# Optimization experiments

Measured on AMD Instinct MI355X. Metric: run time of the kernel, lower is better.

Reference implementation:

```python
import jax, jax.numpy as jnp
import numpy as np
import math

SCALE = 64.0
MARGIN = 0.5
EPS = 1e-07
COS_M = math.cos(MARGIN)
SIN_M = math.sin(MARGIN)
THRESHOLD = math.cos(math.pi - MARGIN)
MM = math.sin(math.pi - MARGIN) * MARGIN

N, D, C = 512, 512, 100000


def setup_inputs() -> dict:
    key = jax.random.key(0)
    k1, k2, k3 = jax.random.split(key, 3)
    x = jax.random.normal(k1, (N, D), dtype=jnp.float32)
    weight = jax.random.normal(k2, (C, D), dtype=jnp.float32)
    t = jnp.zeros((1,), dtype=jnp.float32)
    target = jax.random.randint(k3, (N,), 0, C, dtype=jnp.int64)
    return {"x": x, "weight": weight, "t": t, "target": target}


def reference(x, weight, t, target):
    # normalized linear -> cosine similarities [N, C]
    xn = x / jnp.linalg.norm(x, axis=1, keepdims=True)
    wn = weight / jnp.linalg.norm(weight, axis=1, keepdims=True)
    cos_theta = jnp.clip(jnp.einsum('nd,cd->nc', xn, wn), -1.0 + EPS, 1.0 - EPS)

    rows = jnp.arange(cos_theta.shape[0])
    target_logit = cos_theta[rows, target][:, None]            # [N, 1]
    sin_theta = jnp.sqrt(1.0 - target_logit * target_logit)
    cos_theta_m = target_logit * COS_M - sin_theta * SIN_M      # cos(theta + m)

    mask = cos_theta > cos_theta_m                              # hard examples
    final_target_logit = jnp.where(target_logit > THRESHOLD,
                                   cos_theta_m,
                                   target_logit - MM)

    # EMA buffer update (no-grad in torch)
    t_new = jax.lax.stop_gradient(target_logit.mean() * 0.01 + 0.99 * t)  # [1]

    # hard-example re-weighting: cos * (t + cos) where mask
    cos_theta = jnp.where(mask, cos_theta * (t_new[0] + cos_theta), cos_theta)
    # scatter margin-adjusted target logit into target column
    cos_theta = cos_theta.at[rows, target].set(final_target_logit[:, 0])

    logits = cos_theta * SCALE
    # cross entropy (mean)
    logp = jax.nn.log_softmax(logits, axis=-1)
    loss = -jnp.mean(logp[rows, target])
    return loss
```

## Files before the change

kernel.cpp:

```cpp
#include <hip/hip_runtime.h>
#include <hip/hip_bf16.h>
#include <stdint.h>

#define N_ROWS 512
#define D_DIM  512
#define C_CLS  100000

#define SCALE_F    64.0f
#define EPS_F      1e-7f
#define COS_M_F    0.8775825618903728f
#define SIN_M_F    0.4794255386042030f
#define THRESH_F  -0.8775825618903728f
#define MM_F       0.2397127693021015f
#define FIXMAX_F   65.0f

#define NC  64
#define NG2 1564

#define XN8_OFF    0
#define TL_OFF     (XN8_OFF + 512*512)
#define CTM_OFF    (TL_OFF + 2048)
#define FTL_OFF    (CTM_OFF + 2048)
#define TNEW_OFF   (FTL_OFF + 2048)
#define XNORM_OFF  (TNEW_OFF + 256)
#define PSUM_OFF   (XNORM_OFF + 2048)
#define LOSSI_OFF  (PSUM_OFF + NG2*512*4)

typedef __attribute__((ext_vector_type(4))) float f32x4;

#define GLOAD_LDS16(gp, lp) \
    __builtin_amdgcn_global_load_lds((const __attribute__((address_space(1))) void*)(gp), \
                                     (__attribute__((address_space(3))) void*)(lp), 16, 0, 0)

#if defined(__has_builtin)
#if __has_builtin(__builtin_amdgcn_cvt_pk_fp8_f32)
#define HAVE_CVT_FP8 1
#endif
#endif

__device__ inline unsigned char f2e4m3(float f) {
    union { float f; unsigned u; } a; a.f = f;
    unsigned s = (a.u >> 24) & 0x80u;
    float af = fabsf(f);
    if (af < 0.015625f) {
        int q = (int)(af * 512.0f + 0.5f);
        return (unsigned char)(s | (unsigned)q);
    }
    unsigned x = a.u & 0x7FFFFFFFu;
    unsigned r = x + 0x000FFFFFu + ((x >> 20) & 1u);
    int ec = (int)(r >> 23) - 127 + 7;
    unsigned m = (r >> 20) & 7u;
    if (ec > 15 || (ec == 15 && m == 7u)) return (unsigned char)(s | 0x7Eu);
    return (unsigned char)(s | ((unsigned)ec << 3) | m);
}

__device__ inline unsigned pack4_fp8(float f0, float f1, float f2, float f3) {
#ifdef HAVE_CVT_FP8
    int q = __builtin_amdgcn_cvt_pk_fp8_f32(f0, f1, 0, false);
    q     = __builtin_amdgcn_cvt_pk_fp8_f32(f2, f3, q, true);
    return (unsigned)q;
#else
    union { unsigned char b[4]; unsigned u; } u;
    u.b[0]=f2e4m3(f0); u.b[1]=f2e4m3(f1); u.b[2]=f2e4m3(f2); u.b[3]=f2e4m3(f3);
    return u.u;
#endif
}

__device__ inline uint2 pack8_fp8(float f0, float f1, float f2, float f3,
                                  float f4, float f5, float f6, float f7) {
    uint2 r;
    r.x = pack4_fp8(f0, f1, f2, f3);
    r.y = pack4_fp8(f4, f5, f6, f7);
    return r;
}

__device__ inline float wave_sum64(float v) {
    #pragma unroll
    for (int m = 1; m < 64; m <<= 1) v += __shfl_xor(v, m);
    return v;
}

__global__ void k_xnorm_fp8(const float* __restrict__ x,
                            unsigned char* __restrict__ xn8,
                            float* __restrict__ xnorm) {
    int row = blockIdx.x;
    int lane = threadIdx.x;
    const float* xr = x + row * D_DIM + lane * 8;
    float4 v0 = *(const float4*)(xr);
    float4 v1 = *(const float4*)(xr + 4);
    float s = v0.x*v0.x + v0.y*v0.y + v0.z*v0.z + v0.w*v0.w
            + v1.x*v1.x + v1.y*v1.y + v1.z*v1.z + v1.w*v1.w;
    s = wave_sum64(s);
    float nrm = sqrtf(s);
    if (lane == 0) xnorm[row] = nrm;
    float inv = 1.0f / nrm;
    uint2 q = pack8_fp8(v0.x*inv, v0.y*inv, v0.z*inv, v0.w*inv,
                        v1.x*inv, v1.y*inv, v1.z*inv, v1.w*inv);
    *(uint2*)(xn8 + row * D_DIM + lane * 8) = q;
}

__global__ void k_tlogit(const float* __restrict__ x, const float* __restrict__ w,
                         const float* __restrict__ xnorm,
                         const int* __restrict__ target,
                         float* __restrict__ tl, float* __restrict__ ctm,
                         float* __restrict__ ftl) {
    int row = blockIdx.x;
    int lane = threadIdx.x;
    int tgt = target[row];
    const float* xr = x + row * D_DIM + lane * 8;
    const float* wr = w + (size_t)tgt * D_DIM + lane * 8;
    float4 a0 = *(const float4*)(xr),     a1 = *(const float4*)(xr + 4);
    float4 b0 = *(const float4*)(wr),     b1 = *(const float4*)(wr + 4);
    float s = a0.x*b0.x + a0.y*b0.y + a0.z*b0.z + a0.w*b0.w
            + a1.x*b1.x + a1.y*b1.y + a1.z*b1.z + a1.w*b1.w;
    float q = b0.x*b0.x + b0.y*b0.y + b0.z*b0.z + b0.w*b0.w
            + b1.x*b1.x + b1.y*b1.y + b1.z*b1.z + b1.w*b1.w;
    s = wave_sum64(s);
    q = wave_sum64(q);
    if (lane == 0) {
        float c = s / (xnorm[row] * sqrtf(q));
        c = fminf(fmaxf(c, -1.0f + EPS_F), 1.0f - EPS_F);
        float sn = sqrtf(fmaxf(1.0f - c * c, 0.0f));
        float cm = c * COS_M_F - sn * SIN_M_F;
        tl[row]  = c;
        ctm[row] = cm;
        ftl[row] = (c > THRESH_F) ? cm : (c - MM_F);
    }
}

__global__ void k_tnew(const float* __restrict__ tl, const float* __restrict__ t,
                       float* __restrict__ tnew) {
    __shared__ float s[512];
    int tid = threadIdx.x;
    s[tid] = tl[tid];
    __syncthreads();
    for (int off = 256; off > 0; off >>= 1) {
        if (tid < off) s[tid] += s[tid + off];
        __syncthreads();
    }
    if (tid == 0) tnew[0] = (s[0] / 512.0f) * 0.01f + 0.99f * t[0];
}

__global__ __launch_bounds__(512, 4) void k_fused(
        const unsigned char* __restrict__ xn8,
        const float* __restrict__ w,
        const int* __restrict__ target,
        const float* __restrict__ ctm,
        const float* __restrict__ ftl,
        const float* __restrict__ tnew,
        float* __restrict__ psum) {
    __shared__ unsigned char As[2][512 * 32];
    __shared__ unsigned char Bs[2][64 * 32];
    __shared__ float invS[64];
    __shared__ int   tgt_s[512];
    __shared__ float ctm_s[512];
    __shared__ float ftl_s[512];

    int bx = blockIdx.x;
    int cb = bx * NC;
    int tid = threadIdx.x;
    int lane = tid & 63, wid = tid >> 6;
    int fr = lane & 15, rgrp = lane >> 4;
    int wrow = wid * 64;

    tgt_s[tid] = target[tid];
    ctm_s[tid] = ctm[tid];
    ftl_s[tid] = ftl[tid];
    float tn = tnew[0];

    int brow  = tid >> 3;
    int bslot = tid & 7;
    int bclass = cb + brow;
    bool brvalid = (bclass < C_CLS);
    const float* bsrc = w + (size_t)(brvalid ? bclass : 0) * D_DIM + bslot * 4;

    float sumsq = 0.0f;

    #define STAGE_A(kk, buf)                                                  \
        do {                                                                  \
            _Pragma("unroll")                                                 \
            for (int c = 0; c < 2; ++c) {                                     \
                int lo = c * 8192 + wid * 1024;             \
                int o  = lo + lane * 16;                                      \
                int row = o >> 5, b = o & 31;                                 \
                GLOAD_LDS16(xn8 + (size_t)row * 512 + (kk) * 32 + b,          \
                            (char*)As[buf] + lo);                             \
            }                                                                 \
        } while (0)

    #define WRITE_B(vv, buf)                                                  \
        do {                                                                  \
            sumsq += vv.x*vv.x + vv.y*vv.y + vv.z*vv.z + vv.w*vv.w;           \
            *(unsigned*)(&Bs[buf][brow * 32 + bslot * 4]) =                   \
                pack4_fp8(vv.x, vv.y, vv.z, vv.w);                            \
        } while (0)

    __builtin_amdgcn_sched_barrier(0);
    float4 v0 = *(const float4*)(bsrc);
    STAGE_A(0, 0);
    __builtin_amdgcn_sched_barrier(0);
    float4 rv_next = *(const float4*)(bsrc + 1 * 32);
    float4 rv_far  = *(const float4*)(bsrc + 2 * 32);
    WRITE_B(v0, 0);
    asm volatile("s_waitcnt vmcnt(2) lgkmcnt(0)" ::: "memory");
    __builtin_amdgcn_sched_barrier(0);
    __builtin_amdgcn_s_barrier();
    __builtin_amdgcn_sched_barrier(0);

    f32x4 acc[4][4];
    #pragma unroll
    for (int m = 0; m < 4; m++)
        #pragma unroll
        for (int j = 0; j < 4; j++)
            acc[m][j] = (f32x4){0.f, 0.f, 0.f, 0.f};

    union LL { uint2 u; long long ll; };

    #pragma unroll
    for (int kk = 0; kk < 16; ++kk) {
        int cur = kk & 1;
        if (kk < 15) {
            STAGE_A(kk + 1, cur ^ 1);
            __builtin_amdgcn_sched_barrier(0);
            WRITE_B(rv_next, cur ^ 1);
            rv_next = rv_far;
            if (kk < 13)
                rv_far = *(const float4*)(bsrc + (kk + 3) * 32);
        }
        uint2 af[4], bf[4];
        #pragma unroll
        for (int m = 0; m < 4; m++)
            af[m] = *(const uint2*)(&As[cur][(wrow + m * 16 + fr) * 32 + rgrp * 8]);
        #pragma unroll
        for (int j = 0; j < 4; j++)
            bf[j] = *(const uint2*)(&Bs[cur][(j * 16 + fr) * 32 + rgrp * 8]);
        __builtin_amdgcn_s_setprio(1);
        #pragma unroll
        for (int m = 0; m < 4; m++)
            #pragma unroll
            for (int j = 0; j < 4; j++) {
                LL a, b;
                a.u = af[m];
                b.u = bf[j];
                acc[m][j] = __builtin_amdgcn_mfma_f32_16x16x32_fp8_fp8(
                                a.ll, b.ll, acc[m][j], 0, 0, 0);
            }
        __builtin_amdgcn_s_setprio(0);
        if (kk < 15) {
            if (kk < 13)
                asm volatile("s_waitcnt vmcnt(1) lgkmcnt(0)" ::: "memory");
            else
                asm volatile("s_waitcnt vmcnt(0) lgkmcnt(0)" ::: "memory");
            __builtin_amdgcn_sched_barrier(0);
            __builtin_amdgcn_s_barrier();
            __builtin_amdgcn_sched_barrier(0);
        }
    }
    #undef STAGE_A
    #undef WRITE_B

    float s2 = sumsq;
    s2 += __shfl_xor(s2, 1);
    s2 += __shfl_xor(s2, 2);
    s2 += __shfl_xor(s2, 4);
    if (bslot == 0) invS[brow] = rsqrtf(s2);
    __syncthreads();

    float inv[4];
    bool cvalid[4];
    #pragma unroll
    for (int j = 0; j < 4; j++) {
        inv[j] = invS[j * 16 + fr];
        cvalid[j] = (cb + j * 16 + fr) < C_CLS;
    }
    #pragma unroll
    for (int m = 0; m < 4; m++) {
        #pragma unroll
        for (int reg = 0; reg < 4; reg++) {
            int rl = wrow + m * 16 + rgrp * 4 + reg;
            int tr = tgt_s[rl];
            float cm = ctm_s[rl];
            float ft = ftl_s[rl];
            float sm = 0.0f;
            #pragma unroll
            for (int j = 0; j < 4; j++) {
                int col = cb + j * 16 + fr;
                float c = acc[m][j][reg] * inv[j];
                c = fminf(fmaxf(c, -1.0f + EPS_F), 1.0f - EPS_F);
                float v = (c > cm) ? c * (tn + c) : c;
                v *= SCALE_F;
                v = (col == tr) ? ft * SCALE_F : v;
                v = cvalid[j] ? v : -3.0e38f;
                sm += __expf(v - FIXMAX_F);
            }
            #pragma unroll
            for (int msk = 1; msk < 16; msk <<= 1) sm += __shfl_xor(sm, msk);
            if (fr == 0) psum[(size_t)bx * 512 + rl] = sm;
        }
    }
}

__global__ void k_rowlse_fix(const float* __restrict__ psum,
                             const float* __restrict__ ftl,
                             float* __restrict__ lossi) {
    int row = blockIdx.x, tid = threadIdx.x;
    float S = 0.0f;
    for (int nb = tid; nb < NG2; nb += 256) S += psum[(size_t)nb * 512 + row];
    __shared__ float sS[256];
    sS[tid] = S;
    __syncthreads();
    for (int off = 128; off > 0; off >>= 1) {
        if (tid < off) sS[tid] += sS[tid + off];
        __syncthreads();
    }
    if (tid == 0) lossi[row] = logf(sS[0]) + FIXMAX_F - SCALE_F * ftl[row];
}

__global__ void k_final(const float* __restrict__ lossi, float* __restrict__ out) {
    __shared__ float s[512];
    int tid = threadIdx.x;
    s[tid] = lossi[tid];
    __syncthreads();
    for (int off = 256; off > 0; off >>= 1) {
        if (tid < off) s[tid] += s[tid + off];
        __syncthreads();
    }
    if (tid == 0) out[0] = s[0] / 512.0f;
}

extern "C" void kernel_launch(void* const* d_in, const int* in_sizes, int n_in,
                              void* d_out, int out_size, void* d_ws, size_t ws_size,
                              hipStream_t stream) {
    const float* x      = (const float*)d_in[0];
    const float* w      = (const float*)d_in[1];
    const float* t      = (const float*)d_in[2];
    const int*   target = (const int*)d_in[3];

    char* ws = (char*)d_ws;
    unsigned char* xn8  = (unsigned char*)(ws + XN8_OFF);
    float* tl    = (float*)(ws + TL_OFF);
    float* ctm   = (float*)(ws + CTM_OFF);
    float* ftl   = (float*)(ws + FTL_OFF);
    float* tnew  = (float*)(ws + TNEW_OFF);
    float* xnorm = (float*)(ws + XNORM_OFF);
    float* psum  = (float*)(ws + PSUM_OFF);
    float* lossi = (float*)(ws + LOSSI_OFF);
    float* out   = (float*)d_out;

    k_xnorm_fp8<<<dim3(N_ROWS), dim3(64), 0, stream>>>(x, xn8, xnorm);
    k_tlogit<<<dim3(N_ROWS), dim3(64), 0, stream>>>(x, w, xnorm, target, tl, ctm, ftl);
    k_tnew<<<dim3(1), dim3(512), 0, stream>>>(tl, t, tnew);
    k_fused<<<dim3(NG2), dim3(512), 0, stream>>>(xn8, w, target, ctm, ftl, tnew, psum);
    k_rowlse_fix<<<dim3(N_ROWS), dim3(256), 0, stream>>>(psum, ftl, lossi);
    k_final<<<dim3(1), dim3(512), 0, stream>>>(lossi, out);
}
```

Measured before the change: 122.8 us.

## Double K-tile depth to 64 with XOR-swizzled LDS layout

Each pipeline stage now covers a K slice of 64 instead of 32, which halves the number of main-loop iterations and barriers. A and B tiles in LDS use an XOR swizzle keyed on row to avoid bank conflicts on the wider rows. Each thread loads two float4s of weights per stage, and the vmcnt waits are adjusted to match. LDS usage doubles to about 72KB per block, which may lower occupancy from the requested 4 blocks per CU.

```diff
diff --git a/kernel.cpp b/kernel.cpp
--- a/kernel.cpp
+++ b/kernel.cpp
@@ -149,8 +149,8 @@
         const float* __restrict__ ftl,
         const float* __restrict__ tnew,
         float* __restrict__ psum) {
-    __shared__ unsigned char As[2][512 * 32];
-    __shared__ unsigned char Bs[2][64 * 32];
+    __shared__ unsigned char As[2][512 * 64];
+    __shared__ unsigned char Bs[2][64 * 64];
     __shared__ float invS[64];
     __shared__ int   tgt_s[512];
     __shared__ float ctm_s[512];
@@ -172,37 +172,45 @@
     int bslot = tid & 7;
     int bclass = cb + brow;
     bool brvalid = (bclass < C_CLS);
-    const float* bsrc = w + (size_t)(brvalid ? bclass : 0) * D_DIM + bslot * 4;
+    const float* bsrc = w + (size_t)(brvalid ? bclass : 0) * D_DIM + bslot * 8;
 
     float sumsq = 0.0f;
+    int bwaddr = brow * 64 + ((bslot * 8) ^ ((brow & 3) << 4));
 
     #define STAGE_A(kk, buf)                                                  \
         do {                                                                  \
             _Pragma("unroll")                                                 \
-            for (int c = 0; c < 2; ++c) {                                     \
+            for (int c = 0; c < 4; ++c) {                                     \
                 int lo = c * 8192 + wid * 1024;             \
                 int o  = lo + lane * 16;                                      \
-                int row = o >> 5, b = o & 31;                                 \
-                GLOAD_LDS16(xn8 + (size_t)row * 512 + (kk) * 32 + b,          \
+                int row = o >> 6, b = o & 63;                                 \
+                GLOAD_LDS16(xn8 + (size_t)row * 512 + (kk) * 64               \
+                                + (b ^ ((row & 3) << 4)),                     \
                             (char*)As[buf] + lo);                             \
             }                                                                 \
         } while (0)
 
-    #define WRITE_B(vv, buf)                                                  \
+    #define WRITE_B(va, vb, buf)                                              \
         do {                                                                  \
-            sumsq += vv.x*vv.x + vv.y*vv.y + vv.z*vv.z + vv.w*vv.w;           \
-            *(unsigned*)(&Bs[buf][brow * 32 + bslot * 4]) =                   \
-                pack4_fp8(vv.x, vv.y, vv.z, vv.w);                            \
+            sumsq += va.x*va.x + va.y*va.y + va.z*va.z + va.w*va.w            \
+                   + vb.x*vb.x + vb.y*vb.y + vb.z*vb.z + vb.w*vb.w;           \
+            uint2 pk_;                                                        \
+            pk_.x = pack4_fp8(va.x, va.y, va.z, va.w);                        \
+            pk_.y = pack4_fp8(vb.x, vb.y, vb.z, vb.w);                        \
+            *(uint2*)(&Bs[buf][bwaddr]) = pk_;                                \
         } while (0)
 
     __builtin_amdgcn_sched_barrier(0);
-    float4 v0 = *(const float4*)(bsrc);
+    float4 v0a = *(const float4*)(bsrc);
+    float4 v0b = *(const float4*)(bsrc + 4);
     STAGE_A(0, 0);
     __builtin_amdgcn_sched_barrier(0);
-    float4 rv_next = *(const float4*)(bsrc + 1 * 32);
-    float4 rv_far  = *(const float4*)(bsrc + 2 * 32);
-    WRITE_B(v0, 0);
-    asm volatile("s_waitcnt vmcnt(2) lgkmcnt(0)" ::: "memory");
+    float4 rv_next0 = *(const float4*)(bsrc + 1 * 64);
+    float4 rv_next1 = *(const float4*)(bsrc + 1 * 64 + 4);
+    float4 rv_far0  = *(const float4*)(bsrc + 2 * 64);
+    float4 rv_far1  = *(const float4*)(bsrc + 2 * 64 + 4);
+    WRITE_B(v0a, v0b, 0);
+    asm volatile("s_waitcnt vmcnt(4) lgkmcnt(0)" ::: "memory");
     __builtin_amdgcn_sched_barrier(0);
     __builtin_amdgcn_s_barrier();
     __builtin_amdgcn_sched_barrier(0);
@@ -215,40 +223,48 @@
             acc[m][j] = (f32x4){0.f, 0.f, 0.f, 0.f};
 
     union LL { uint2 u; long long ll; };
-
-    #pragma unroll
-    for (int kk = 0; kk < 16; ++kk) {
+    int akey = (fr & 3) << 4;
+
+    #pragma unroll
+    for (int kk = 0; kk < 8; ++kk) {
         int cur = kk & 1;
-        if (kk < 15) {
+        if (kk < 7) {
             STAGE_A(kk + 1, cur ^ 1);
             __builtin_amdgcn_sched_barrier(0);
-            WRITE_B(rv_next, cur ^ 1);
-            rv_next = rv_far;
-            if (kk < 13)
-                rv_far = *(const float4*)(bsrc + (kk + 3) * 32);
+            WRITE_B(rv_next0, rv_next1, cur ^ 1);
+            rv_next0 = rv_far0;
+            rv_next1 = rv_far1;
+            if (kk < 5) {
+                rv_far0 = *(const float4*)(bsrc + (kk + 3) * 64);
+                rv_far1 = *(const float4*)(bsrc + (kk + 3) * 64 + 4);
+            }
         }
-        uint2 af[4], bf[4];
         #pragma unroll
-        for (int m = 0; m < 4; m++)
-            af[m] = *(const uint2*)(&As[cur][(wrow + m * 16 + fr) * 32 + rgrp * 8]);
-        #pragma unroll
-        for (int j = 0; j < 4; j++)
-            bf[j] = *(const uint2*)(&Bs[cur][(j * 16 + fr) * 32 + rgrp * 8]);
-        __builtin_amdgcn_s_setprio(1);
-        #pragma unroll
-        for (int m = 0; m < 4; m++)
-            #pragma unroll
-            for (int j = 0; j < 4; j++) {
-                LL a, b;
-                a.u = af[m];
-                b.u = bf[j];
-                acc[m][j] = __builtin_amdgcn_mfma_f32_16x16x32_fp8_fp8(
-                                a.ll, b.ll, acc[m][j], 0, 0, 0);
-            }
-        __builtin_amdgcn_s_setprio(0);
-        if (kk < 15) {
-            if (kk < 13)
-                asm volatile("s_waitcnt vmcnt(1) lgkmcnt(0)" ::: "memory");
+        for (int sub = 0; sub < 2; ++sub) {
+            uint2 af[4], bf[4];
+            int soff = (sub * 32 + rgrp * 8) ^ akey;
+            #pragma unroll
+            for (int m = 0; m < 4; m++)
+                af[m] = *(const uint2*)(&As[cur][(wrow + m * 16 + fr) * 64 + soff]);
+            #pragma unroll
+            for (int j = 0; j < 4; j++)
+                bf[j] = *(const uint2*)(&Bs[cur][(j * 16 + fr) * 64 + soff]);
+            __builtin_amdgcn_s_setprio(1);
+            #pragma unroll
+            for (int m = 0; m < 4; m++)
+                #pragma unroll
+                for (int j = 0; j < 4; j++) {
+                    LL a, b;
+                    a.u = af[m];
+                    b.u = bf[j];
+                    acc[m][j] = __builtin_amdgcn_mfma_f32_16x16x32_fp8_fp8(
+                                    a.ll, b.ll, acc[m][j], 0, 0, 0);
+                }
+            __builtin_amdgcn_s_setprio(0);
+        }
+        if (kk < 7) {
+            if (kk < 5)
+                asm volatile("s_waitcnt vmcnt(2) lgkmcnt(0)" ::: "memory");
             else
                 asm volatile("s_waitcnt vmcnt(0) lgkmcnt(0)" ::: "memory");
             __builtin_amdgcn_sched_barrier(0);
```

Result: no change. 122.8 us (-0.0%).
